# Performance work log

Measured on AMD Instinct MI355X. Metric: run time of the kernel, lower is better.

The kernel has to match this reference:

```python
import jax, jax.numpy as jnp
import numpy as np

B, S, HID = 2, 2048, 2048
H = 16
HD = HID // H            # 128
HD2 = HD // 2            # 64 (rope dim per head)
LAT = HID // 8           # 256 latent dim
BASE = 10000.0


def _rotary_table(seq_len):
    # inv_freq over rope dim HD2
    inv_freq = 1.0 / (BASE ** (jnp.arange(0, HD2, 2, dtype=jnp.float32) / HD2))  # [HD2//2]
    pos = jnp.arange(seq_len, dtype=jnp.float32)
    sincos = pos[:, None] * inv_freq[None, :]                 # [S, HD2//2]
    return jnp.concatenate([jnp.sin(sincos), jnp.cos(sincos)], axis=-1)  # [S, HD2]


def _apply_rope(x, emb):
    # x: [B, S, H, HD2]; emb: [S, HD2]
    half = HD2 // 2
    x1, x2 = x[..., :half], x[..., half:]
    sin = emb[None, :, None, :half]
    cos = emb[None, :, None, half:]
    return jnp.concatenate([x1 * cos - x2 * sin, x1 * sin + x2 * cos], axis=-1)


def setup_inputs() -> dict:
    key = jax.random.key(0)
    ks = jax.random.split(key, 9)
    s = 0.02
    return {
        "hidden_states": jax.random.normal(ks[0], (B, S, HID), jnp.float32),
        "w_kv_d": jax.random.normal(ks[1], (HID, LAT), jnp.float32) * s,
        "w_q_d": jax.random.normal(ks[2], (HID, LAT), jnp.float32) * s,
        "w_k_u": jax.random.normal(ks[3], (LAT, H * HD2), jnp.float32) * s,
        "w_q_u": jax.random.normal(ks[4], (LAT, H * HD2), jnp.float32) * s,
        "w_v_u": jax.random.normal(ks[5], (LAT, H * HD), jnp.float32) * s,
        "w_rope_k": jax.random.normal(ks[6], (HID, HID // 2), jnp.float32) * s,
        "w_rope_q": jax.random.normal(ks[7], (LAT, HID // 2), jnp.float32) * s,
        "w_o": jax.random.normal(ks[8], (HID, HID), jnp.float32) * s,
    }


def reference(hidden_states, w_kv_d, w_q_d, w_k_u, w_q_u, w_v_u, w_rope_k, w_rope_q, w_o):
    b, s, _ = hidden_states.shape
    kv_d = hidden_states @ w_kv_d            # [B,S,LAT]
    q_d = hidden_states @ w_q_d              # [B,S,LAT]
    k_p = (kv_d @ w_k_u).reshape(b, s, H, HD2)
    q_p = (q_d @ w_q_u).reshape(b, s, H, HD2)
    v = (kv_d @ w_v_u).reshape(b, s, H, HD)
    k_r = (hidden_states @ w_rope_k).reshape(b, s, H, HD2)
    q_r = (q_d @ w_rope_q).reshape(b, s, H, HD2)

    emb = _rotary_table(s)
    k_r = _apply_rope(k_r, emb)
    q_r = _apply_rope(q_r, emb)

    k = jnp.concatenate([k_p, k_r], axis=-1)  # [B,S,H,HD]
    q = jnp.concatenate([q_p, q_r], axis=-1)

    scores = jnp.einsum('bqhd,bkhd->bhqk', q, k) / jnp.sqrt(jnp.float32(HD))
    causal = jnp.tril(jnp.ones((s, s), dtype=bool))
    scores = jnp.where(causal[None, None], scores, jnp.float32(-1e9))
    probs = jax.nn.softmax(scores, axis=-1)
    out = jnp.einsum('bhqk,bkhd->bqhd', probs, v).reshape(b, s, HID)
    return out @ w_o
```

## Files before the change

kernel.cpp:

```cpp
#include <hip/hip_runtime.h>
#include <hip/hip_bf16.h>

#define BB 2
#define SS 2048
#define HID 2048
#define NH 16
#define BS (BB*SS)
#define SCALE 0.088388347648318447f
#define C2LOG 0.12751743f

typedef __bf16 bf16x8 __attribute__((ext_vector_type(8)));
typedef float f32x4 __attribute__((ext_vector_type(4)));
typedef float f32x16 __attribute__((ext_vector_type(16)));
typedef unsigned int uintx2 __attribute__((ext_vector_type(2)));

__device__ __forceinline__ bf16x8 ld_frag(const __hip_bfloat16* p) {
    uint4 u = *reinterpret_cast<const uint4*>(p);
    return __builtin_bit_cast(bf16x8, u);
}
__device__ __forceinline__ unsigned int cvt_pk_bf16(float a, float b) {
    unsigned int r;
    asm("v_cvt_pk_bf16_f32 %0, %1, %2" : "=v"(r) : "v"(a), "v"(b));
    return r;
}
__device__ __forceinline__ ushort bf_bits(float v) {
    return (ushort)cvt_pk_bf16(v, v);
}
__device__ __forceinline__ void store_c(__hip_bfloat16* C, size_t idx, float v) {
    *reinterpret_cast<ushort*>(&C[idx]) = bf_bits(v);
}
__device__ __forceinline__ void store_c(float* C, size_t idx, float v) {
    C[idx] = v;
}

#define GLD16(gp, lp) \
  __builtin_amdgcn_global_load_lds((const __attribute__((address_space(1))) void*)(gp), \
                                   (__attribute__((address_space(3))) void*)(lp), 16, 0, 0)


__global__ __launch_bounds__(256) void convert_kernel(
    const float* __restrict__ src, __hip_bfloat16* __restrict__ dst, int n8)
{
    int i = blockIdx.x * blockDim.x + threadIdx.x;
    if (i >= n8) return;
    float4 a = reinterpret_cast<const float4*>(src)[2 * i];
    float4 b = reinterpret_cast<const float4*>(src)[2 * i + 1];
    uint4 o;
    o.x = cvt_pk_bf16(a.x, a.y);
    o.y = cvt_pk_bf16(a.z, a.w);
    o.z = cvt_pk_bf16(b.x, b.y);
    o.w = cvt_pk_bf16(b.z, b.w);
    reinterpret_cast<uint4*>(dst)[i] = o;
}

__global__ __launch_bounds__(256) void transpose_weights_kernel(
    const float* s0, const float* s1, const float* s2, const float* s3,
    const float* s4, const float* s5, const float* s6, const float* s7,
    __hip_bfloat16* WT1, __hip_bfloat16* WT2, __hip_bfloat16* WT3,
    __hip_bfloat16* WTo)
{
    const float* srcs[8] = { s0, s1, s2, s3, s4, s5, s6, s7 };
    const int Rs[8] = { 2048, 2048, 2048, 256, 256, 256, 256, 2048 };
    const int Cs[8] = { 256, 256, 1024, 1024, 2048, 1024, 1024, 2048 };
    __hip_bfloat16* dsts[8] = {
        WT1, WT1 + (size_t)256 * 2048, WT1 + (size_t)512 * 2048,
        WT2, WT2 + (size_t)1024 * 256,
        WT3, WT3 + (size_t)1024 * 256,
        WTo };
    const int prefix[9] = { 0, 512, 1024, 3072, 3328, 3840, 4096, 4352, 8448 };

    int bid = blockIdx.x;
    int seg = 0;
    #pragma unroll
    for (int i = 0; i < 8; i++) if (bid >= prefix[i + 1]) seg = i + 1;
    int local = bid - prefix[seg];
    int R = Rs[seg], C = Cs[seg];
    int tilesC = C / 32;
    int tr = local / tilesC, tc = local % tilesC;
    int r0 = tr * 32, c0 = tc * 32;
    const float* src = srcs[seg];
    __hip_bfloat16* dst = dsts[seg];

    __shared__ float Ts[32][33];
    int t = threadIdx.x;
    int ty = t >> 5, tx = t & 31;
    #pragma unroll
    for (int k = 0; k < 4; k++) {
        int r = ty + k * 8;
        Ts[r][tx] = src[(size_t)(r0 + r) * C + c0 + tx];
    }
    __syncthreads();
    #pragma unroll
    for (int k = 0; k < 4; k++) {
        int r = ty + k * 8;
        *reinterpret_cast<ushort*>(&dst[(size_t)(c0 + r) * R + r0 + tx]) =
            bf_bits(Ts[tx][r]);
    }
}

template <typename TC>
__global__ __launch_bounds__(256) void gemm_bt_kernel(
    const __hip_bfloat16* __restrict__ A, int lda,
    const __hip_bfloat16* __restrict__ Bt,
    TC* __restrict__ C0, int ldc0, int sp0, int off0, float cm0,
    TC* __restrict__ C1, int ldc1, int sp1, int off1, float cm1,
    int splitN, int K)
{
    __shared__ alignas(16) __hip_bfloat16 As[128 * 32];
    __shared__ alignas(16) __hip_bfloat16 Bs[128 * 32];

    const int nwg = gridDim.x * gridDim.y;
    int lin = blockIdx.y * gridDim.x + blockIdx.x;
    lin = (lin & 7) * (nwg >> 3) + (lin >> 3);
    const int bn = (lin % gridDim.x) * 128;
    const int bm = (lin / gridDim.x) * 128;

    const int t = threadIdx.x;
    const int w = t >> 6;
    const int lane = t & 63;
    const int l15 = lane & 15;
    const int quad = lane >> 4;
    const int wm = (w & 1) * 64;
    const int wn = (w >> 1) * 64;

    const int srow = lane >> 2;
    const int skcol = (lane & 3) * 8;

    f32x4 acc[4][4] = {};

    for (int k0 = 0; k0 < K; k0 += 32) {
        __syncthreads();
        #pragma unroll
        for (int i = 0; i < 2; i++) {
            int r = w * 32 + i * 16 + srow;
            GLD16(A + (size_t)(bm + r) * lda + k0 + skcol, &As[r * 32 + skcol]);
            GLD16(Bt + (size_t)(bn + r) * K + k0 + skcol, &Bs[r * 32 + skcol]);
        }
        __syncthreads();

        bf16x8 af[4], bf[4];
        #pragma unroll
        for (int mt = 0; mt < 4; mt++)
            af[mt] = ld_frag(&As[(wm + mt * 16 + l15) * 32 + quad * 8]);
        #pragma unroll
        for (int nt = 0; nt < 4; nt++)
            bf[nt] = ld_frag(&Bs[(wn + nt * 16 + l15) * 32 + quad * 8]);
        #pragma unroll
        for (int mt = 0; mt < 4; mt++)
            #pragma unroll
            for (int nt = 0; nt < 4; nt++)
                acc[mt][nt] = __builtin_amdgcn_mfma_f32_16x16x32_bf16(
                    af[mt], bf[nt], acc[mt][nt], 0, 0, 0);
    }

    #pragma unroll
    for (int nt = 0; nt < 4; nt++) {
        int col = bn + wn + nt * 16 + l15;
        TC* Cp; int c, ld, s64, off; float cm;
        if (col < splitN) { Cp = C0; c = col; ld = ldc0; s64 = sp0; off = off0; cm = cm0; }
        else { Cp = C1; c = col - splitN; ld = ldc1; s64 = sp1; off = off1; cm = cm1; }
        if (s64 == 2) {
            #pragma unroll
            for (int mt = 0; mt < 4; mt++) {
                int row0 = bm + wm + mt * 16 + quad * 4;
                #pragma unroll
                for (int r = 0; r < 4; r++)
                    store_c(Cp, (size_t)c * 4096 + row0 + r, acc[mt][nt][r] * cm);
            }
        } else if (s64 == 3) {
            const int hh = c >> 6, d = off + (c & 63);
            const size_t dbase = (size_t)(d >> 4) * 512
                               + (size_t)((d >> 3) & 1) * 256 + (d & 7);
            #pragma unroll
            for (int mt = 0; mt < 4; mt++) {
                #pragma unroll
                for (int r = 0; r < 4; r++) {
                    int m = bm + wm + mt * 16 + quad * 4 + r;
                    int bb2 = m >> 11, kv = m & 2047;
                    size_t idx = (size_t)(bb2 * 16 + hh) * 262144
                               + (size_t)(kv >> 5) * 4096 + dbase
                               + (size_t)(kv & 31) * 8;
                    store_c(Cp, idx, acc[mt][nt][r] * cm);
                }
            }
        } else if (s64 == 4) {
            const int hh = c >> 7, d = c & 127;
            const size_t dbase = (size_t)(d >> 5) * 2048 + (size_t)(d & 31) * 8;
            #pragma unroll
            for (int mt = 0; mt < 4; mt++) {
                #pragma unroll
                for (int r = 0; r < 4; r++) {
                    int m = bm + wm + mt * 16 + quad * 4 + r;
                    int bb2 = m >> 11, kv = m & 2047;
                    size_t idx = (size_t)(bb2 * 16 + hh) * 262144
                               + (size_t)(kv >> 6) * 8192 + dbase
                               + (size_t)((kv >> 4) & 3) * 512
                               + (size_t)((kv >> 3) & 1) * 256 + (kv & 7);
                    store_c(Cp, idx, acc[mt][nt][r] * cm);
                }
            }
        } else {
            int oc = s64 ? ((c >> 6) * 128 + (c & 63) + off) : c;
            #pragma unroll
            for (int mt = 0; mt < 4; mt++) {
                #pragma unroll
                for (int r = 0; r < 4; r++) {
                    int row = bm + wm + mt * 16 + quad * 4 + r;
                    store_c(Cp, (size_t)row * ld + oc, acc[mt][nt][r] * cm);
                }
            }
        }
    }
}

__global__ __launch_bounds__(256) void rope_kernel(
    __hip_bfloat16* __restrict__ Kf, __hip_bfloat16* __restrict__ Qb)
{
    int idx = blockIdx.x * blockDim.x + threadIdx.x;
    if (idx >= BS * NH * 32) return;
    int i = idx & 31;
    int h = (idx >> 5) & 15;
    int row = idx >> 9;
    int s = row & (SS - 1);
    int b = row >> 11;

    float inv = exp2f(-(float)i * 0.4152410118609203f);
    float ang = (float)s * inv;
    float sn = sinf(ang), cs = cosf(ang);

    {
        size_t kaddr = ((size_t)(b * 16 + h) * 64 + (s >> 5)) * 4096
                     + (size_t)(4 + (i >> 4)) * 512
                     + (size_t)(((i >> 3) & 1) * 32 + (s & 31)) * 8 + (i & 7);
        float x1 = __bfloat162float(Kf[kaddr]);
        float x2 = __bfloat162float(Kf[kaddr + 1024]);
        *reinterpret_cast<ushort*>(&Kf[kaddr])        = bf_bits(x1 * cs - x2 * sn);
        *reinterpret_cast<ushort*>(&Kf[kaddr + 1024]) = bf_bits(x1 * sn + x2 * cs);
    }
    {
        size_t obase = (size_t)row * 2048 + h * 128 + 64 + i;
        float x1 = __bfloat162float(Qb[obase]);
        float x2 = __bfloat162float(Qb[obase + 32]);
        *reinterpret_cast<ushort*>(&Qb[obase])      = bf_bits(x1 * cs - x2 * sn);
        *reinterpret_cast<ushort*>(&Qb[obase + 32]) = bf_bits(x1 * sn + x2 * cs);
    }
}

__global__ __launch_bounds__(512) void flash_attn_kernel(
    const __hip_bfloat16* __restrict__ Q,
    const __hip_bfloat16* __restrict__ Kf,
    const __hip_bfloat16* __restrict__ Vf,
    __hip_bfloat16* __restrict__ O)
{
    __shared__ alignas(16) __hip_bfloat16 Ktd[2 * 16 * 512];
    __shared__ alignas(16) __hip_bfloat16 Vsd[2 * 16 * 512];

    const int p = blockIdx.x;
    const int h = blockIdx.y;
    const int b = blockIdx.z;
    const int t = threadIdx.x;
    const int w = t >> 6;
    const int lane = t & 63;
    const int l31 = lane & 31;
    const int hi = lane >> 5;

    const int qt = (w < 4) ? (15 - p) : p;
    const int wq = w & 3;
    const int qwb = qt * 128 + wq * 32;
    const int q = qwb + l31;
    const int my_nt = 2 * qt + 1 + (wq >> 1);
    const int nbig = 2 * (15 - p) + 2;

    const __hip_bfloat16* Kfb = Kf + (size_t)(b * 16 + h) * 262144;
    const __hip_bfloat16* Vfb = Vf + (size_t)(b * 16 + h) * 262144;

    bf16x8 qf[8];
    {
        const __hip_bfloat16* qrow = Q + (size_t)(b * SS + q) * 2048 + h * 128;
        #pragma unroll
        for (int s = 0; s < 8; s++)
            qf[s] = ld_frag(qrow + s * 16 + hi * 8);
    }

    const int kreg = (w & 1) * 8 + (w >> 1) * 2;
    const int loff = lane * 8;
    const __hip_bfloat16* kp = Kfb + (size_t)((w & 1) * 4096 + (w >> 1) * 1024) + loff;
    const __hip_bfloat16* vp = Vfb + (size_t)(2 * w) * 512 + loff;
    __hip_bfloat16* kd[2] = { &Ktd[kreg * 512 + loff], &Ktd[8192 + kreg * 512 + loff] };
    __hip_bfloat16* vd[2] = { &Vsd[2 * w * 512 + loff], &Vsd[8192 + 2 * w * 512 + loff] };

    float m_i = -INFINITY;
    float l_i = 0.0f;
    f32x16 acc[4] = {};

    GLD16(kp, kd[0]);
    GLD16(kp + 512, kd[0] + 512);
    GLD16(vp, vd[0]);
    GLD16(vp + 512, vd[0] + 512);
    kp += 8192; vp += 8192;
    asm volatile("" :: "v"(qf[0]), "v"(qf[1]), "v"(qf[2]), "v"(qf[3]),
                       "v"(qf[4]), "v"(qf[5]), "v"(qf[6]), "v"(qf[7]));

    for (int kt = 0; kt < nbig; kt++) {
        const int kvb = kt * 64;
        const int par = kt & 1;
        const bool active = (kt < my_nt);

        asm volatile("s_waitcnt vmcnt(0)" ::: "memory");
        __builtin_amdgcn_s_barrier();
        asm volatile("" ::: "memory");

        {
            const int pn = par ^ 1;
            GLD16(kp, kd[pn]);
            GLD16(kp + 512, kd[pn] + 512);
            GLD16(vp, vd[pn]);
            GLD16(vp + 512, vd[pn] + 512);
            if (kt + 2 < nbig) { kp += 8192; vp += 8192; }
        }

        if (active) {
            const __hip_bfloat16* kb_base = &Ktd[par * 8192];
            const __hip_bfloat16* vb_base = &Vsd[par * 8192];

            f32x16 st[2] = {};
            __builtin_amdgcn_s_setprio(1);
            #pragma unroll
            for (int s = 0; s < 8; s++)
                #pragma unroll
                for (int kb = 0; kb < 2; kb++) {
                    bf16x8 kf = ld_frag(kb_base + (kb * 8 + s) * 512 + loff);
                    st[kb] = __builtin_amdgcn_mfma_f32_32x32x16_bf16(
                        kf, qf[s], st[kb], 0, 0, 0);
                }
            __builtin_amdgcn_s_setprio(0);

            float tmx;
            if (kvb + 63 > qwb) {
                const int thr = q - kvb - 4 * hi;
                tmx = -INFINITY;
                #pragma unroll
                for (int kb = 0; kb < 2; kb++)
                    #pragma unroll
                    for (int g = 0; g < 4; g++)
                        #pragma unroll
                        for (int r = 0; r < 4; r++) {
                            const int e = g * 4 + r;
                            float v = (kb * 32 + 8 * g + r <= thr) ? st[kb][e] : -INFINITY;
                            st[kb][e] = v;
                            tmx = fmaxf(tmx, v);
                        }
            } else {
                tmx = fmaxf(st[0][0], st[0][1]);
                #pragma unroll
                for (int e = 2; e < 16; e += 2)
                    tmx = fmaxf(fmaxf(tmx, st[0][e]), st[0][e + 1]);
                #pragma unroll
                for (int e = 0; e < 16; e += 2)
                    tmx = fmaxf(fmaxf(tmx, st[1][e]), st[1][e + 1]);
            }
            tmx = fmaxf(tmx, __shfl_xor(tmx, 32));
            const float m2x = tmx * C2LOG;

            const bool nosc = __all(m2x <= m_i + 8.0f);
            const float mnew = nosc ? m_i : fmaxf(m_i, m2x);
            float rs = 0.0f;
            #pragma unroll
            for (int kb = 0; kb < 2; kb++)
                #pragma unroll
                for (int e = 0; e < 16; e++) {
                    float pv = exp2f(fmaf(st[kb][e], C2LOG, -mnew));
                    st[kb][e] = pv;
                    rs += pv;
                }
            rs += __shfl_xor(rs, 32);
            if (!nosc) {
                const float alpha = exp2f(m_i - mnew);
                m_i = mnew;
                l_i *= alpha;
                #pragma unroll
                for (int dt = 0; dt < 4; dt++)
                    #pragma unroll
                    for (int e = 0; e < 16; e++)
                        acc[dt][e] *= alpha;
            }
            l_i += rs;

            uint4 af[4];
            #pragma unroll
            for (int kb = 0; kb < 2; kb++) {
                unsigned int pk[4][2];
                #pragma unroll
                for (int g = 0; g < 4; g++)
                    #pragma unroll
                    for (int i = 0; i < 2; i++)
                        pk[g][i] = cvt_pk_bf16(st[kb][g * 4 + 2 * i],
                                               st[kb][g * 4 + 2 * i + 1]);
                #pragma unroll
                for (int sl = 0; sl < 2; sl++) {
                    uintx2 r0 = __builtin_amdgcn_permlane32_swap(
                        pk[2 * sl][0], pk[2 * sl + 1][0], false, false);
                    uintx2 r1 = __builtin_amdgcn_permlane32_swap(
                        pk[2 * sl][1], pk[2 * sl + 1][1], false, false);
                    af[kb * 2 + sl] = make_uint4(r0[0], r1[0], r0[1], r1[1]);
                }
            }

            __builtin_amdgcn_s_setprio(1);
            #pragma unroll
            for (int s = 0; s < 4; s++) {
                bf16x8 pf = __builtin_bit_cast(bf16x8, af[s]);
                #pragma unroll
                for (int dt = 0; dt < 4; dt++) {
                    bf16x8 vf = ld_frag(vb_base + (dt * 4 + s) * 512 + loff);
                    acc[dt] = __builtin_amdgcn_mfma_f32_32x32x16_bf16(
                        vf, pf, acc[dt], 0, 0, 0);
                }
            }
            __builtin_amdgcn_s_setprio(0);
        }
    }

    const float inv_l = 1.0f / l_i;
    __hip_bfloat16* orow = O + (size_t)(b * SS + q) * 2048 + h * 128;
    #pragma unroll
    for (int dt = 0; dt < 4; dt++)
        #pragma unroll
        for (int g = 0; g < 4; g++) {
            uint2 uu;
            uu.x = cvt_pk_bf16(acc[dt][g * 4 + 0] * inv_l, acc[dt][g * 4 + 1] * inv_l);
            uu.y = cvt_pk_bf16(acc[dt][g * 4 + 2] * inv_l, acc[dt][g * 4 + 3] * inv_l);
            *reinterpret_cast<uint2*>(orow + dt * 32 + 8 * g + 4 * hi) = uu;
        }
}

extern "C" void kernel_launch(void* const* d_in, const int* in_sizes, int n_in,
                              void* d_out, int out_size, void* d_ws, size_t ws_size,
                              hipStream_t stream)
{
    const float* hs       = (const float*)d_in[0];
    const float* w_kv_d   = (const float*)d_in[1];
    const float* w_q_d    = (const float*)d_in[2];
    const float* w_k_u    = (const float*)d_in[3];
    const float* w_q_u    = (const float*)d_in[4];
    const float* w_v_u    = (const float*)d_in[5];
    const float* w_rope_k = (const float*)d_in[6];
    const float* w_rope_q = (const float*)d_in[7];
    const float* w_o      = (const float*)d_in[8];
    float* out = (float*)d_out;

    char* p = (char*)d_ws;
    auto alloc = [&](size_t nelem) {
        __hip_bfloat16* r = (__hip_bfloat16*)p;
        p += nelem * sizeof(__hip_bfloat16);
        return r;
    };
    __hip_bfloat16* hsb  = alloc((size_t)BS * HID);
    __hip_bfloat16* qkvd = alloc((size_t)BS * 512);
    __hip_bfloat16* WT1  = alloc((size_t)1536 * 2048);
    __hip_bfloat16* WT2  = alloc((size_t)3072 * 256);
    __hip_bfloat16* WT3  = alloc((size_t)2048 * 256);
    __hip_bfloat16* WTo  = alloc((size_t)2048 * 2048);
    __hip_bfloat16* Kf   = alloc((size_t)BS * HID);
    __hip_bfloat16* Qbuf = alloc((size_t)BS * HID);
    __hip_bfloat16* Vf   = alloc((size_t)HID * BS);
    __hip_bfloat16* attn = hsb;

    dim3 blk(256);

    convert_kernel<<<dim3((BS * HID / 8 + 255) / 256), blk, 0, stream>>>(
        hs, hsb, BS * HID / 8);
    transpose_weights_kernel<<<dim3(8448), blk, 0, stream>>>(
        w_kv_d, w_q_d, w_rope_k, w_k_u, w_v_u, w_q_u, w_rope_q, w_o,
        WT1, WT2, WT3, WTo);

    gemm_bt_kernel<__hip_bfloat16><<<dim3(1536 / 128, BS / 128), blk, 0, stream>>>(
        hsb, 2048, WT1,
        qkvd, 512, 0, 0, 1.0f,
        Kf, 0, 3, 64, 1.0f,
        512, 2048);
    gemm_bt_kernel<__hip_bfloat16><<<dim3(3072 / 128, BS / 128), blk, 0, stream>>>(
        qkvd, 512, WT2,
        Kf, 0, 3, 0, 1.0f,
        Vf, 0, 4, 0, 1.0f,
        1024, 256);
    gemm_bt_kernel<__hip_bfloat16><<<dim3(2048 / 128, BS / 128), blk, 0, stream>>>(
        qkvd + 256, 512, WT3,
        Qbuf, 2048, 1, 0, 1.0f,
        Qbuf, 2048, 1, 64, 1.0f,
        1024, 256);
    rope_kernel<<<dim3((BS * NH * 32 + 255) / 256), blk, 0, stream>>>(Kf, Qbuf);
    flash_attn_kernel<<<dim3(8, NH, BB), dim3(512), 0, stream>>>(
        Qbuf, Kf, Vf, attn);
    gemm_bt_kernel<float><<<dim3(2048 / 128, BS / 128), blk, 0, stream>>>(
        attn, 2048, WTo,
        out, 2048, 0, 0, 1.0f,
        out, 2048, 0, 0, 1.0f,
        2048, 2048);
}
```

Baseline: 336.5 us.

## Triple-buffer K/V tiles in flash attention and remap grid for head locality

Moves the K/V shared-memory staging in the flash attention kernel from double to triple buffering. Two tiles are prefetched up front and the wait becomes vmcnt(4), so one tile's loads can still be in flight during compute. The block index mapping also changes so that blockIdx.x spans heads, which alters scheduling order and possibly L2 locality. In exchange, shared memory per block grows from 64KB to 96KB, which may cut occupancy, and the launch grid must match the new mapping.

```diff
diff --git a/kernel.cpp b/kernel.cpp
--- a/kernel.cpp
+++ b/kernel.cpp
@@ -252,11 +252,11 @@
     const __hip_bfloat16* __restrict__ Vf,
     __hip_bfloat16* __restrict__ O)
 {
-    __shared__ alignas(16) __hip_bfloat16 Ktd[2 * 16 * 512];
-    __shared__ alignas(16) __hip_bfloat16 Vsd[2 * 16 * 512];
-
-    const int p = blockIdx.x;
-    const int h = blockIdx.y;
+    __shared__ alignas(16) __hip_bfloat16 Ktd[3 * 16 * 512];
+    __shared__ alignas(16) __hip_bfloat16 Vsd[3 * 16 * 512];
+
+    const int p = blockIdx.y & 7;
+    const int h = blockIdx.x + 8 * (blockIdx.y >> 3);
     const int b = blockIdx.z;
     const int t = threadIdx.x;
     const int w = t >> 6;
@@ -282,46 +282,48 @@
             qf[s] = ld_frag(qrow + s * 16 + hi * 8);
     }
 
-    const int kreg = (w & 1) * 8 + (w >> 1) * 2;
     const int loff = lane * 8;
-    const __hip_bfloat16* kp = Kfb + (size_t)((w & 1) * 4096 + (w >> 1) * 1024) + loff;
-    const __hip_bfloat16* vp = Vfb + (size_t)(2 * w) * 512 + loff;
-    __hip_bfloat16* kd[2] = { &Ktd[kreg * 512 + loff], &Ktd[8192 + kreg * 512 + loff] };
-    __hip_bfloat16* vd[2] = { &Vsd[2 * w * 512 + loff], &Vsd[8192 + 2 * w * 512 + loff] };
+    const size_t kwoff = (size_t)((w & 1) * 4096 + (w >> 1) * 1024) + loff;
+    const size_t vwoff = (size_t)(2 * w) * 512 + loff;
+    const int kroff = ((w & 1) * 8 + (w >> 1) * 2) * 512 + loff;
+    const int vroff = 2 * w * 512 + loff;
 
     float m_i = -INFINITY;
     float l_i = 0.0f;
     f32x16 acc[4] = {};
 
-    GLD16(kp, kd[0]);
-    GLD16(kp + 512, kd[0] + 512);
-    GLD16(vp, vd[0]);
-    GLD16(vp + 512, vd[0] + 512);
-    kp += 8192; vp += 8192;
+    GLD16(Kfb + kwoff,       &Ktd[kroff]);
+    GLD16(Kfb + kwoff + 512, &Ktd[kroff + 512]);
+    GLD16(Vfb + vwoff,       &Vsd[vroff]);
+    GLD16(Vfb + vwoff + 512, &Vsd[vroff + 512]);
+    GLD16(Kfb + 8192 + kwoff,       &Ktd[8192 + kroff]);
+    GLD16(Kfb + 8192 + kwoff + 512, &Ktd[8192 + kroff + 512]);
+    GLD16(Vfb + 8192 + vwoff,       &Vsd[8192 + vroff]);
+    GLD16(Vfb + 8192 + vwoff + 512, &Vsd[8192 + vroff + 512]);
     asm volatile("" :: "v"(qf[0]), "v"(qf[1]), "v"(qf[2]), "v"(qf[3]),
                        "v"(qf[4]), "v"(qf[5]), "v"(qf[6]), "v"(qf[7]));
 
+    int cb = 0, sb = 2;
     for (int kt = 0; kt < nbig; kt++) {
         const int kvb = kt * 64;
-        const int par = kt & 1;
         const bool active = (kt < my_nt);
 
-        asm volatile("s_waitcnt vmcnt(0)" ::: "memory");
+        asm volatile("s_waitcnt vmcnt(4)" ::: "memory");
         __builtin_amdgcn_s_barrier();
         asm volatile("" ::: "memory");
 
         {
-            const int pn = par ^ 1;
-            GLD16(kp, kd[pn]);
-            GLD16(kp + 512, kd[pn] + 512);
-            GLD16(vp, vd[pn]);
-            GLD16(vp + 512, vd[pn] + 512);
-            if (kt + 2 < nbig) { kp += 8192; vp += 8192; }
+            const size_t soff = (size_t)((kt + 2 < nbig) ? kt + 2 : nbig - 1) * 8192;
+            const int sl = sb * 8192;
+            GLD16(Kfb + soff + kwoff,       &Ktd[sl + kroff]);
+            GLD16(Kfb + soff + kwoff + 512, &Ktd[sl + kroff + 512]);
+            GLD16(Vfb + soff + vwoff,       &Vsd[sl + vroff]);
+            GLD16(Vfb + soff + vwoff + 512, &Vsd[sl + vroff + 512]);
         }
 
         if (active) {
-            const __hip_bfloat16* kb_base = &Ktd[par * 8192];
-            const __hip_bfloat16* vb_base = &Vsd[par * 8192];
+            const __hip_bfloat16* kb_base = &Ktd[cb * 8192];
+            const __hip_bfloat16* vb_base = &Vsd[cb * 8192];
 
             f32x16 st[2] = {};
             __builtin_amdgcn_s_setprio(1);
@@ -419,6 +421,9 @@
             }
             __builtin_amdgcn_s_setprio(0);
         }
+
+        cb = (cb == 2) ? 0 : cb + 1;
+        sb = (sb == 2) ? 0 : sb + 1;
     }
 
     const float inv_l = 1.0f / l_i;
```

Result: slower. 346.2 us (+2.9%).
